# Kernel tuning notes

Measured on AMD Instinct MI355X. Metric: run time of the kernel, lower is better.

Reference implementation:

```python
import jax, jax.numpy as jnp
import numpy as np

N_HEAD = 16
D_HEAD = 64
D_MODEL = 1024
LN_EPS = 1e-5


def layer_norm(x, gamma, beta):
    mu = jnp.mean(x, axis=-1, keepdims=True)
    var = jnp.mean((x - mu) ** 2, axis=-1, keepdims=True)
    return (x - mu) * jax.lax.rsqrt(var + LN_EPS) * gamma + beta


def setup_inputs() -> dict:
    key = jax.random.key(0)
    ks = jax.random.split(key, 6)
    B, T = 2, 2048
    inp = jax.random.normal(ks[0], (B, T, D_MODEL), dtype=jnp.float32)
    # qkv_net: Linear(d_model, 3*n_head*d_head)
    W_qkv = jax.random.normal(ks[1], (3 * N_HEAD * D_HEAD, D_MODEL), dtype=jnp.float32) * (D_MODEL ** -0.5)
    b_qkv = jax.random.normal(ks[2], (3 * N_HEAD * D_HEAD,), dtype=jnp.float32) * 0.02
    # o_net: Linear(n_head*d_head, d_model, bias=False)
    W_o = jax.random.normal(ks[3], (D_MODEL, N_HEAD * D_HEAD), dtype=jnp.float32) * ((N_HEAD * D_HEAD) ** -0.5)
    gamma = jnp.ones((D_MODEL,), dtype=jnp.float32)
    beta = jnp.zeros((D_MODEL,), dtype=jnp.float32)
    return {"inp": inp, "W_qkv": W_qkv, "b_qkv": b_qkv, "W_o": W_o, "gamma": gamma, "beta": beta}


def reference(inp, W_qkv, b_qkv, W_o, gamma, beta):
    B, T, D = inp.shape
    H, dh = N_HEAD, D_HEAD
    scale = 1.0 / (dh ** 0.5)

    qkv = inp @ W_qkv.T + b_qkv                      # (B, T, 3*H*dh)
    head_q, head_k, head_v = jnp.split(qkv, 3, axis=2)
    # (B, T, H, dh) -> (B, H, T, dh)
    q = head_q.reshape(B, T, H, dh).transpose(0, 2, 1, 3)
    k = head_k.reshape(B, T, H, dh).transpose(0, 2, 1, 3)
    v = head_v.reshape(B, T, H, dh).transpose(0, 2, 1, 3)

    attn_score = jnp.einsum('bhqd,bhkd->bhqk', q, k) * scale  # (B, H, T, T)
    attn_prob = jax.nn.softmax(attn_score, axis=-1)           # dropatt is identity in eval
    attn_vec = jnp.einsum('bhqk,bhkd->bhqd', attn_prob, v)    # (B, H, T, dh)

    # Faithful to original: (B*H, T, dh) batch-major buffer is VIEWED as (H, B, T, dh)
    attn_vec = attn_vec.reshape(H, B, T, dh)
    attn_vec = attn_vec.transpose(1, 2, 0, 3).reshape(B, T, H * dh)

    attn_out = attn_vec @ W_o.T                                # dropout identity in eval
    return layer_norm(inp + attn_out, gamma, beta)
```

## Files before the change

### kernel.cpp

```cpp
#include <hip/hip_runtime.h>
#include <hip/hip_bf16.h>
#include <stdint.h>

typedef __bf16 bf16_t;
typedef __bf16 bf16x8 __attribute__((ext_vector_type(8)));
typedef __bf16 bf16x4 __attribute__((ext_vector_type(4)));
typedef float floatx4 __attribute__((ext_vector_type(4)));

#define QSCALE 0.180336879f

__device__ static inline void gll16(const void* g, void* l) {
    __builtin_amdgcn_global_load_lds((const __attribute__((address_space(1))) void*)g,
                                     (__attribute__((address_space(3))) void*)l, 16, 0, 0);
}

__global__ __launch_bounds__(256) void cvt_all(const float* __restrict__ inp,
                                               const float* __restrict__ wqkv,
                                               const float* __restrict__ wo,
                                               bf16_t* __restrict__ o_inp,
                                               bf16_t* __restrict__ o_wqkv,
                                               bf16_t* __restrict__ o_wo) {
    int blk = blockIdx.x;
    const float* src;
    bf16_t* dst;
    if (blk < 4096)      { src = inp;  dst = o_inp; }
    else if (blk < 7168) { src = wqkv; dst = o_wqkv; blk -= 4096; }
    else                 { src = wo;   dst = o_wo;   blk -= 7168; }
    int i = blk * 256 + threadIdx.x;
    float4 v = ((const float4*)src)[i];
    bf16x4 o;
    o[0] = (bf16_t)v.x; o[1] = (bf16_t)v.y; o[2] = (bf16_t)v.z; o[3] = (bf16_t)v.w;
    ((bf16x4*)dst)[i] = o;
}

__global__ __launch_bounds__(256, 3)
void gemm_qkv(const bf16_t* __restrict__ A, const bf16_t* __restrict__ Bw,
              const float* __restrict__ bias,
              bf16_t* __restrict__ qk, bf16_t* __restrict__ vT) {
    constexpr int K = 1024;
    __shared__ bf16_t lA[128 * 32];
    __shared__ bf16_t lB[128 * 32];
    const int tid  = threadIdx.x;
    const int lane = tid & 63, wave = tid >> 6;
    const int quad = lane >> 4, l16 = lane & 15;
    const int wy = wave >> 1, wx = wave & 1;
    const int bm = blockIdx.y * 128, bn = blockIdx.x * 128;

    const int c0 = tid, c1 = tid + 256;
    const bf16_t* Ap0 = A + (size_t)(bm + (c0 >> 2)) * K + (c0 & 3) * 8;
    const bf16_t* Ap1 = A + (size_t)(bm + (c1 >> 2)) * K + (c1 & 3) * 8;
    const bf16_t* Bp0 = Bw + (size_t)(bn + (c0 >> 2)) * K + (c0 & 3) * 8;
    const bf16_t* Bp1 = Bw + (size_t)(bn + (c1 >> 2)) * K + (c1 & 3) * 8;
    bf16_t* dA0 = &lA[(wave * 64) * 8];
    bf16_t* dA1 = &lA[(256 + wave * 64) * 8];
    bf16_t* dB0 = &lB[(wave * 64) * 8];
    bf16_t* dB1 = &lB[(256 + wave * 64) * 8];

    floatx4 acc[4][4] = {};

    for (int kt = 0; kt < K; kt += 32) {
        __syncthreads();
        gll16(Ap0 + kt, dA0);
        gll16(Ap1 + kt, dA1);
        gll16(Bp0 + kt, dB0);
        gll16(Bp1 + kt, dB1);
        __syncthreads();
        bf16x8 af[4], bfr[4];
#pragma unroll
        for (int i = 0; i < 4; i++) {
            af[i]  = *(const bf16x8*)(lA + (wy * 64 + i * 16 + l16) * 32 + quad * 8);
            bfr[i] = *(const bf16x8*)(lB + (wx * 64 + i * 16 + l16) * 32 + quad * 8);
        }
#pragma unroll
        for (int i = 0; i < 4; i++)
#pragma unroll
            for (int j = 0; j < 4; j++)
                acc[i][j] = __builtin_amdgcn_mfma_f32_16x16x32_bf16(af[i], bfr[j], acc[i][j], 0, 0, 0);
    }

    const bool is_v = (bn >= 2048);
#pragma unroll
    for (int j = 0; j < 4; j++) {
        const int n = bn + wx * 64 + j * 16 + l16;
        const float bv = bias[n];
        const bool isq = (n < 1024);
#pragma unroll
        for (int i = 0; i < 4; i++) {
            const int mbase = bm + wy * 64 + i * 16 + quad * 4;
            if (!is_v) {
#pragma unroll
                for (int r = 0; r < 4; r++) {
                    float c = acc[i][j][r] + bv;
                    if (isq) c *= QSCALE;
                    qk[(size_t)(mbase + r) * 2048 + n] = (bf16_t)c;
                }
            } else {
                const int nn = n - 2048;
                const int b  = mbase >> 11;
                const int t  = mbase & 2047;
                const int vrow = b * 1024 + nn;
                bf16x4 pack;
#pragma unroll
                for (int r = 0; r < 4; r++) pack[r] = (bf16_t)(acc[i][j][r] + bv);
                *(bf16x4*)(vT + (size_t)vrow * 2048 + t) = pack;
            }
        }
    }
}

__global__ __launch_bounds__(256, 3)
void attn_kernel(const bf16_t* __restrict__ qk, const bf16_t* __restrict__ vT,
                 bf16_t* __restrict__ av) {
    __shared__ bf16_t Kbuf[2][2][64 * 32];
    __shared__ bf16_t Vbuf[2][2][64 * 32];
    __shared__ bf16_t Pbuf[4][2][16 * 32];
    const int tid  = threadIdx.x;
    const int lane = tid & 63, wave = tid >> 6;
    const int quad = lane >> 4, l16 = lane & 15;
    const int bid = blockIdx.x;
    const int s  = bid & 31;
    const int hl = (s & 7) * 4 + (s >> 3);
    const int qt = bid >> 5;
    const int b = hl >> 4, h = hl & 15;

    const bf16_t* Qbase = qk + (size_t)(b * 2048 + qt * 128 + wave * 32) * 2048 + h * 64;
    const bf16_t* Kbase = qk + (size_t)(b * 2048) * 2048 + 1024 + h * 64;
    const bf16_t* Vbase = vT + (size_t)(hl * 64) * 2048;

    const int sr = tid >> 3;
    const int c8 = tid & 7;
    const int half = c8 >> 2, ce = (c8 & 3) * 8;
    const bf16_t* Kg = Kbase + (size_t)sr * 2048 + c8 * 8;
    const bf16_t* Vg = Vbase + (size_t)sr * 2048 + c8 * 8;

    bf16x8 qf[2][2];
#pragma unroll
    for (int rt = 0; rt < 2; rt++)
#pragma unroll
        for (int kc = 0; kc < 2; kc++)
            qf[rt][kc] = *(const bf16x8*)(Qbase + (size_t)(rt * 16 + l16) * 2048 + kc * 32 + quad * 8);

    floatx4 accO[2][4] = {};
    float lacc[2] = {0.f, 0.f};

    {
        bf16x8 k0 = *(const bf16x8*)(Kg);
        bf16x8 k1 = *(const bf16x8*)(Kg + (size_t)32 * 2048);
        bf16x8 v0 = *(const bf16x8*)(Vg);
        bf16x8 v1 = *(const bf16x8*)(Vg + (size_t)32 * 2048);
        *(bf16x8*)&Kbuf[0][half][sr * 32 + ce] = k0;
        *(bf16x8*)&Kbuf[0][half][(sr + 32) * 32 + ce] = k1;
        *(bf16x8*)&Vbuf[0][half][sr * 32 + ce] = v0;
        *(bf16x8*)&Vbuf[0][half][(sr + 32) * 32 + ce] = v1;
    }

    for (int it = 0; it < 32; ++it) {
        const int cur = it & 1;
        __syncthreads();
        bf16x8 gk0, gk1, gv0, gv1;
        if (it < 31) {
            const bf16_t* kg = Kg + (size_t)(it + 1) * 64 * 2048;
            const bf16_t* vg = Vg + (it + 1) * 64;
            gk0 = *(const bf16x8*)(kg);
            gk1 = *(const bf16x8*)(kg + (size_t)32 * 2048);
            gv0 = *(const bf16x8*)(vg);
            gv1 = *(const bf16x8*)(vg + (size_t)32 * 2048);
        }
        floatx4 st[2][4] = {};
#pragma unroll
        for (int nt = 0; nt < 4; nt++) {
            bf16x8 k0 = *(const bf16x8*)&Kbuf[cur][0][(nt * 16 + l16) * 32 + quad * 8];
            bf16x8 k1 = *(const bf16x8*)&Kbuf[cur][1][(nt * 16 + l16) * 32 + quad * 8];
            st[0][nt] = __builtin_amdgcn_mfma_f32_16x16x32_bf16(k0, qf[0][0], st[0][nt], 0, 0, 0);
            st[0][nt] = __builtin_amdgcn_mfma_f32_16x16x32_bf16(k1, qf[0][1], st[0][nt], 0, 0, 0);
            st[1][nt] = __builtin_amdgcn_mfma_f32_16x16x32_bf16(k0, qf[1][0], st[1][nt], 0, 0, 0);
            st[1][nt] = __builtin_amdgcn_mfma_f32_16x16x32_bf16(k1, qf[1][1], st[1][nt], 0, 0, 0);
        }
#pragma unroll
        for (int rt = 0; rt < 2; rt++) {
            float ls = 0.f;
#pragma unroll
            for (int nt = 0; nt < 4; nt++) {
                bf16x4 pk;
#pragma unroll
                for (int r = 0; r < 4; r++) {
                    float p = __builtin_amdgcn_exp2f(st[rt][nt][r]);
                    ls += p;
                    pk[r] = (bf16_t)p;
                }
                *(bf16x4*)&Pbuf[wave][nt >> 1][l16 * 32 + (nt & 1) * 16 + quad * 4] = pk;
            }
            lacc[rt] += ls;
        }
#pragma unroll
        for (int kc2 = 0; kc2 < 2; kc2++) {
            bf16x8 pf0 = *(const bf16x8*)&Pbuf[wave][kc2][l16 * 32 + quad * 8];
            pf0 = pf0;
            break;
        }
        {
#pragma unroll
            for (int rt = 0; rt < 2; rt++) {
#pragma unroll
                for (int nt = 0; nt < 4; nt++) {
                    bf16x4 pk;
#pragma unroll
                    for (int r = 0; r < 4; r++)
                        pk[r] = (bf16_t)__builtin_amdgcn_exp2f(st[rt][nt][r]);
                    *(bf16x4*)&Pbuf[wave][nt >> 1][l16 * 32 + (nt & 1) * 16 + quad * 4] = pk;
                }
#pragma unroll
                for (int kc2 = 0; kc2 < 2; kc2++) {
                    bf16x8 pf = *(const bf16x8*)&Pbuf[wave][kc2][l16 * 32 + quad * 8];
#pragma unroll
                    for (int ct = 0; ct < 4; ct++) {
                        bf16x8 vf = *(const bf16x8*)&Vbuf[cur][kc2][(ct * 16 + l16) * 32 + quad * 8];
                        accO[rt][ct] = __builtin_amdgcn_mfma_f32_16x16x32_bf16(pf, vf, accO[rt][ct], 0, 0, 0);
                    }
                }
            }
        }
        if (it < 31) {
            const int nxt = cur ^ 1;
            *(bf16x8*)&Kbuf[nxt][half][sr * 32 + ce] = gk0;
            *(bf16x8*)&Kbuf[nxt][half][(sr + 32) * 32 + ce] = gk1;
            *(bf16x8*)&Vbuf[nxt][half][sr * 32 + ce] = gv0;
            *(bf16x8*)&Vbuf[nxt][half][(sr + 32) * 32 + ce] = gv1;
        }
    }

    float linv[2];
#pragma unroll
    for (int rt = 0; rt < 2; rt++) {
        float l = lacc[rt];
        l += __shfl_xor(l, 16);
        l += __shfl_xor(l, 32);
        linv[rt] = 1.0f / l;
    }
    const int b2 = hl & 1;
    const int colb = (hl >> 1) * 64;
    bf16_t* outb = av + (size_t)(b2 * 2048 + qt * 128 + wave * 32) * 1024 + colb;
#pragma unroll
    for (int rt = 0; rt < 2; rt++) {
        float invq[4];
#pragma unroll
        for (int r = 0; r < 4; r++) invq[r] = __shfl(linv[rt], quad * 4 + r);
#pragma unroll
        for (int ct = 0; ct < 4; ct++)
#pragma unroll
            for (int r = 0; r < 4; r++)
                outb[(size_t)(rt * 16 + quad * 4 + r) * 1024 + ct * 16 + l16] =
                    (bf16_t)(accO[rt][ct][r] * invq[r]);
    }
}

__global__ __launch_bounds__(256, 4)
void gemm_o(const bf16_t* __restrict__ A, const bf16_t* __restrict__ Bw,
            float* __restrict__ out) {
    constexpr int K = 1024;
    __shared__ bf16_t lA[64 * 32];
    __shared__ bf16_t lB[128 * 32];
    const int tid  = threadIdx.x;
    const int lane = tid & 63, wave = tid >> 6;
    const int quad = lane >> 4, l16 = lane & 15;
    const int wy = wave >> 1, wx = wave & 1;
    const int bm = blockIdx.y * 64, bn = blockIdx.x * 128;

    const int ca = tid;
    const int cb0 = tid, cb1 = tid + 256;
    const bf16_t* Ap  = A + (size_t)(bm + (ca >> 2)) * K + (ca & 3) * 8;
    const bf16_t* Bp0 = Bw + (size_t)(bn + (cb0 >> 2)) * K + (cb0 & 3) * 8;
    const bf16_t* Bp1 = Bw + (size_t)(bn + (cb1 >> 2)) * K + (cb1 & 3) * 8;
    bf16_t* dA  = &lA[(wave * 64) * 8];
    bf16_t* dB0 = &lB[(wave * 64) * 8];
    bf16_t* dB1 = &lB[(256 + wave * 64) * 8];

    floatx4 acc[2][4] = {};
    for (int kt = 0; kt < K; kt += 32) {
        __syncthreads();
        gll16(Ap + kt, dA);
        gll16(Bp0 + kt, dB0);
        gll16(Bp1 + kt, dB1);
        __syncthreads();
        bf16x8 af[2], bfr[4];
#pragma unroll
        for (int i = 0; i < 2; i++)
            af[i] = *(const bf16x8*)(lA + (wy * 32 + i * 16 + l16) * 32 + quad * 8);
#pragma unroll
        for (int j = 0; j < 4; j++)
            bfr[j] = *(const bf16x8*)(lB + (wx * 64 + j * 16 + l16) * 32 + quad * 8);
#pragma unroll
        for (int i = 0; i < 2; i++)
#pragma unroll
            for (int j = 0; j < 4; j++)
                acc[i][j] = __builtin_amdgcn_mfma_f32_16x16x32_bf16(af[i], bfr[j], acc[i][j], 0, 0, 0);
    }
#pragma unroll
    for (int j = 0; j < 4; j++) {
        const int n = bn + wx * 64 + j * 16 + l16;
#pragma unroll
        for (int i = 0; i < 2; i++) {
            const int mbase = bm + wy * 32 + i * 16 + quad * 4;
#pragma unroll
            for (int r = 0; r < 4; r++)
                out[(size_t)(mbase + r) * 1024 + n] = acc[i][j][r];
        }
    }
}

__global__ __launch_bounds__(256)
void ln_kernel(const float* __restrict__ inp, const float* __restrict__ ao,
               const float* __restrict__ gamma, const float* __restrict__ beta,
               float* __restrict__ out) {
    const int row = blockIdx.x, tid = threadIdx.x;
    const int wave = tid >> 6, lane = tid & 63;
    float4 a = ((const float4*)(inp + (size_t)row * 1024))[tid];
    float4 c = ((const float4*)(ao + (size_t)row * 1024))[tid];
    float x0 = a.x + c.x, x1 = a.y + c.y, x2 = a.z + c.z, x3 = a.w + c.w;
    float s = x0 + x1 + x2 + x3;
    float sq = x0 * x0 + x1 * x1 + x2 * x2 + x3 * x3;
#pragma unroll
    for (int mm = 32; mm >= 1; mm >>= 1) {
        s += __shfl_xor(s, mm);
        sq += __shfl_xor(sq, mm);
    }
    __shared__ float rs[4], rq[4];
    if (lane == 0) { rs[wave] = s; rq[wave] = sq; }
    __syncthreads();
    s = rs[0] + rs[1] + rs[2] + rs[3];
    sq = rq[0] + rq[1] + rq[2] + rq[3];
    const float mu = s * (1.0f / 1024.0f);
    const float var = sq * (1.0f / 1024.0f) - mu * mu;
    const float rstd = rsqrtf(var + 1e-5f);
    float4 g = ((const float4*)gamma)[tid], bt = ((const float4*)beta)[tid];
    float4 o;
    o.x = (x0 - mu) * rstd * g.x + bt.x;
    o.y = (x1 - mu) * rstd * g.y + bt.y;
    o.z = (x2 - mu) * rstd * g.z + bt.z;
    o.w = (x3 - mu) * rstd * g.w + bt.w;
    ((float4*)(out + (size_t)row * 1024))[tid] = o;
}

extern "C" void kernel_launch(void* const* d_in, const int* in_sizes, int n_in,
                              void* d_out, int out_size, void* d_ws, size_t ws_size,
                              hipStream_t stream) {
    const float* inp   = (const float*)d_in[0];
    const float* Wqkv  = (const float*)d_in[1];
    const float* bqkv  = (const float*)d_in[2];
    const float* Wo    = (const float*)d_in[3];
    const float* gamma = (const float*)d_in[4];
    const float* beta  = (const float*)d_in[5];
    float* out = (float*)d_out;

    char* ws = (char*)d_ws;
    bf16_t* inp_bf  = (bf16_t*)(ws);
    bf16_t* wqkv_bf = (bf16_t*)(ws + (8u << 20));
    bf16_t* wo_bf   = (bf16_t*)(ws + (14u << 20));
    bf16_t* qk_buf  = (bf16_t*)(ws + (16u << 20));
    bf16_t* vT_buf  = (bf16_t*)(ws + (32u << 20));
    bf16_t* av_buf  = (bf16_t*)(ws + (40u << 20));
    float*  ao_buf  = (float*)(ws + (48u << 20));

    cvt_all<<<8192, 256, 0, stream>>>(inp, Wqkv, Wo, inp_bf, wqkv_bf, wo_bf);
    gemm_qkv<<<dim3(24, 32), 256, 0, stream>>>(inp_bf, wqkv_bf, bqkv, qk_buf, vT_buf);
    attn_kernel<<<512, 256, 0, stream>>>(qk_buf, vT_buf, av_buf);
    gemm_o<<<dim3(8, 64), 256, 0, stream>>>(av_buf, wo_bf, ao_buf);
    ln_kernel<<<4096, 256, 0, stream>>>(inp, ao_buf, gamma, beta, out);
}
```

Before: 210.4 us.

## Split attention over key halves with global_load_lds staging and combine kernel

The attention kernel now splits the key dimension into two halves, doubling the grid to 1024 blocks. Each block writes an unnormalized partial output and row sums, and a new combine kernel adds the halves and normalizes. K/V tiles are staged with direct global-to-LDS loads instead of register round-trips, the duplicated exp/P recomputation is removed, and the occupancy hint is raised to 4. The cost is an extra kernel launch plus partial-buffer traffic, and workspace regions are reused (lpart over inp_bf, opart over ao_buf).

```diff
diff --git a/kernel.cpp b/kernel.cpp
--- a/kernel.cpp
+++ b/kernel.cpp
@@ -108,30 +108,33 @@
     }
 }
 
-__global__ __launch_bounds__(256, 3)
+__global__ __launch_bounds__(256, 4)
 void attn_kernel(const bf16_t* __restrict__ qk, const bf16_t* __restrict__ vT,
-                 bf16_t* __restrict__ av) {
-    __shared__ bf16_t Kbuf[2][2][64 * 32];
-    __shared__ bf16_t Vbuf[2][2][64 * 32];
-    __shared__ bf16_t Pbuf[4][2][16 * 32];
+                 bf16_t* __restrict__ Opart, float* __restrict__ lpart) {
+    __shared__ bf16_t Kbuf[2][64 * 64];
+    __shared__ bf16_t Vbuf[2][64 * 64];
+    __shared__ bf16_t Pbuf[4][16 * 32];
     const int tid  = threadIdx.x;
     const int lane = tid & 63, wave = tid >> 6;
     const int quad = lane >> 4, l16 = lane & 15;
     const int bid = blockIdx.x;
-    const int s  = bid & 31;
-    const int hl = (s & 7) * 4 + (s >> 3);
-    const int qt = bid >> 5;
+    const int s    = bid & 63;
+    const int hl   = ((s & 7) << 2) | ((s >> 3) & 3);
+    const int half = (s >> 5) & 1;
+    const int qt   = bid >> 6;
     const int b = hl >> 4, h = hl & 15;
+    const int kt0 = half * 1024;
 
     const bf16_t* Qbase = qk + (size_t)(b * 2048 + qt * 128 + wave * 32) * 2048 + h * 64;
     const bf16_t* Kbase = qk + (size_t)(b * 2048) * 2048 + 1024 + h * 64;
     const bf16_t* Vbase = vT + (size_t)(hl * 64) * 2048;
 
-    const int sr = tid >> 3;
-    const int c8 = tid & 7;
-    const int half = c8 >> 2, ce = (c8 & 3) * 8;
-    const bf16_t* Kg = Kbase + (size_t)sr * 2048 + c8 * 8;
-    const bf16_t* Vg = Vbase + (size_t)sr * 2048 + c8 * 8;
+    const int srow = tid >> 2, sc8 = (tid & 3) * 8;
+    const bf16_t* KgA = Kbase + (size_t)(kt0 + srow) * 2048 + sc8;
+    const bf16_t* KgB = KgA + 32;
+    const bf16_t* VgA = Vbase + (size_t)srow * 2048 + kt0 + sc8;
+    const bf16_t* VgB = VgA + 32;
+    const int wbase = wave * 512;
 
     bf16x8 qf[2][2];
 #pragma unroll
@@ -143,115 +146,102 @@
     floatx4 accO[2][4] = {};
     float lacc[2] = {0.f, 0.f};
 
-    {
-        bf16x8 k0 = *(const bf16x8*)(Kg);
-        bf16x8 k1 = *(const bf16x8*)(Kg + (size_t)32 * 2048);
-        bf16x8 v0 = *(const bf16x8*)(Vg);
-        bf16x8 v1 = *(const bf16x8*)(Vg + (size_t)32 * 2048);
-        *(bf16x8*)&Kbuf[0][half][sr * 32 + ce] = k0;
-        *(bf16x8*)&Kbuf[0][half][(sr + 32) * 32 + ce] = k1;
-        *(bf16x8*)&Vbuf[0][half][sr * 32 + ce] = v0;
-        *(bf16x8*)&Vbuf[0][half][(sr + 32) * 32 + ce] = v1;
-    }
-
-    for (int it = 0; it < 32; ++it) {
-        const int cur = it & 1;
-        __syncthreads();
-        bf16x8 gk0, gk1, gv0, gv1;
-        if (it < 31) {
-            const bf16_t* kg = Kg + (size_t)(it + 1) * 64 * 2048;
-            const bf16_t* vg = Vg + (it + 1) * 64;
-            gk0 = *(const bf16x8*)(kg);
-            gk1 = *(const bf16x8*)(kg + (size_t)32 * 2048);
-            gv0 = *(const bf16x8*)(vg);
-            gv1 = *(const bf16x8*)(vg + (size_t)32 * 2048);
+    gll16(KgA, &Kbuf[0][wbase]);
+    gll16(KgB, &Kbuf[0][2048 + wbase]);
+    gll16(VgA, &Vbuf[0][wbase]);
+    gll16(VgB, &Vbuf[0][2048 + wbase]);
+
+    for (int it = 0; it < 16; ++it) {
+        const int cur = it & 1, nxt = cur ^ 1;
+        __syncthreads();
+        if (it < 15) {
+            const size_t ko = (size_t)(it + 1) * 64 * 2048;
+            const int    vo = (it + 1) * 64;
+            gll16(KgA + ko, &Kbuf[nxt][wbase]);
+            gll16(KgB + ko, &Kbuf[nxt][2048 + wbase]);
+            gll16(VgA + vo, &Vbuf[nxt][wbase]);
+            gll16(VgB + vo, &Vbuf[nxt][2048 + wbase]);
         }
         floatx4 st[2][4] = {};
 #pragma unroll
         for (int nt = 0; nt < 4; nt++) {
-            bf16x8 k0 = *(const bf16x8*)&Kbuf[cur][0][(nt * 16 + l16) * 32 + quad * 8];
-            bf16x8 k1 = *(const bf16x8*)&Kbuf[cur][1][(nt * 16 + l16) * 32 + quad * 8];
+            bf16x8 k0 = *(const bf16x8*)&Kbuf[cur][(nt * 16 + l16) * 32 + quad * 8];
+            bf16x8 k1 = *(const bf16x8*)&Kbuf[cur][2048 + (nt * 16 + l16) * 32 + quad * 8];
             st[0][nt] = __builtin_amdgcn_mfma_f32_16x16x32_bf16(k0, qf[0][0], st[0][nt], 0, 0, 0);
             st[0][nt] = __builtin_amdgcn_mfma_f32_16x16x32_bf16(k1, qf[0][1], st[0][nt], 0, 0, 0);
             st[1][nt] = __builtin_amdgcn_mfma_f32_16x16x32_bf16(k0, qf[1][0], st[1][nt], 0, 0, 0);
             st[1][nt] = __builtin_amdgcn_mfma_f32_16x16x32_bf16(k1, qf[1][1], st[1][nt], 0, 0, 0);
         }
 #pragma unroll
-        for (int rt = 0; rt < 2; rt++) {
-            float ls = 0.f;
-#pragma unroll
-            for (int nt = 0; nt < 4; nt++) {
-                bf16x4 pk;
-#pragma unroll
-                for (int r = 0; r < 4; r++) {
-                    float p = __builtin_amdgcn_exp2f(st[rt][nt][r]);
-                    ls += p;
-                    pk[r] = (bf16_t)p;
+        for (int kc2 = 0; kc2 < 2; kc2++) {
+            bf16x8 vf[4];
+#pragma unroll
+            for (int ct = 0; ct < 4; ct++)
+                vf[ct] = *(const bf16x8*)&Vbuf[cur][kc2 * 2048 + (ct * 16 + l16) * 32 + quad * 8];
+#pragma unroll
+            for (int rt = 0; rt < 2; rt++) {
+                float ls = 0.f;
+#pragma unroll
+                for (int ntl = 0; ntl < 2; ntl++) {
+                    const floatx4 sv = st[rt][kc2 * 2 + ntl];
+                    bf16x4 pk;
+#pragma unroll
+                    for (int r = 0; r < 4; r++) {
+                        float p = __builtin_amdgcn_exp2f(sv[r]);
+                        ls += p;
+                        pk[r] = (bf16_t)p;
+                    }
+                    *(bf16x4*)&Pbuf[wave][l16 * 32 + ntl * 16 + quad * 4] = pk;
                 }
-                *(bf16x4*)&Pbuf[wave][nt >> 1][l16 * 32 + (nt & 1) * 16 + quad * 4] = pk;
+                lacc[rt] += ls;
+                bf16x8 pf = *(const bf16x8*)&Pbuf[wave][l16 * 32 + quad * 8];
+#pragma unroll
+                for (int ct = 0; ct < 4; ct++)
+                    accO[rt][ct] = __builtin_amdgcn_mfma_f32_16x16x32_bf16(pf, vf[ct], accO[rt][ct], 0, 0, 0);
             }
-            lacc[rt] += ls;
-        }
-#pragma unroll
-        for (int kc2 = 0; kc2 < 2; kc2++) {
-            bf16x8 pf0 = *(const bf16x8*)&Pbuf[wave][kc2][l16 * 32 + quad * 8];
-            pf0 = pf0;
-            break;
-        }
-        {
-#pragma unroll
-            for (int rt = 0; rt < 2; rt++) {
-#pragma unroll
-                for (int nt = 0; nt < 4; nt++) {
-                    bf16x4 pk;
-#pragma unroll
-                    for (int r = 0; r < 4; r++)
-                        pk[r] = (bf16_t)__builtin_amdgcn_exp2f(st[rt][nt][r]);
-                    *(bf16x4*)&Pbuf[wave][nt >> 1][l16 * 32 + (nt & 1) * 16 + quad * 4] = pk;
-                }
-#pragma unroll
-                for (int kc2 = 0; kc2 < 2; kc2++) {
-                    bf16x8 pf = *(const bf16x8*)&Pbuf[wave][kc2][l16 * 32 + quad * 8];
-#pragma unroll
-                    for (int ct = 0; ct < 4; ct++) {
-                        bf16x8 vf = *(const bf16x8*)&Vbuf[cur][kc2][(ct * 16 + l16) * 32 + quad * 8];
-                        accO[rt][ct] = __builtin_amdgcn_mfma_f32_16x16x32_bf16(pf, vf, accO[rt][ct], 0, 0, 0);
-                    }
-                }
-            }
-        }
-        if (it < 31) {
-            const int nxt = cur ^ 1;
-            *(bf16x8*)&Kbuf[nxt][half][sr * 32 + ce] = gk0;
-            *(bf16x8*)&Kbuf[nxt][half][(sr + 32) * 32 + ce] = gk1;
-            *(bf16x8*)&Vbuf[nxt][half][sr * 32 + ce] = gv0;
-            *(bf16x8*)&Vbuf[nxt][half][(sr + 32) * 32 + ce] = gv1;
-        }
-    }
-
-    float linv[2];
+        }
+    }
+
+    float lsum[2];
 #pragma unroll
     for (int rt = 0; rt < 2; rt++) {
         float l = lacc[rt];
         l += __shfl_xor(l, 16);
         l += __shfl_xor(l, 32);
-        linv[rt] = 1.0f / l;
+        lsum[rt] = l;
     }
     const int b2 = hl & 1;
-    const int colb = (hl >> 1) * 64;
-    bf16_t* outb = av + (size_t)(b2 * 2048 + qt * 128 + wave * 32) * 1024 + colb;
-#pragma unroll
-    for (int rt = 0; rt < 2; rt++) {
-        float invq[4];
-#pragma unroll
-        for (int r = 0; r < 4; r++) invq[r] = __shfl(linv[rt], quad * 4 + r);
+    const int colb = hl >> 1;
+    const int rowb = b2 * 2048 + qt * 128 + wave * 32;
+    bf16_t* outb = Opart + (size_t)half * (4096 * 1024) + (size_t)rowb * 1024 + colb * 64;
+#pragma unroll
+    for (int rt = 0; rt < 2; rt++)
 #pragma unroll
         for (int ct = 0; ct < 4; ct++)
 #pragma unroll
             for (int r = 0; r < 4; r++)
-                outb[(size_t)(rt * 16 + quad * 4 + r) * 1024 + ct * 16 + l16] =
-                    (bf16_t)(accO[rt][ct][r] * invq[r]);
-    }
+                outb[(size_t)(rt * 16 + quad * 4 + r) * 1024 + ct * 16 + l16] = (bf16_t)(accO[rt][ct][r]);
+    if (quad == 0) {
+#pragma unroll
+        for (int rt = 0; rt < 2; rt++)
+            lpart[half * 65536 + (rowb + rt * 16 + l16) * 16 + colb] = lsum[rt];
+    }
+}
+
+__global__ __launch_bounds__(256)
+void attn_combine(const bf16_t* __restrict__ Op, const float* __restrict__ lp,
+                  bf16_t* __restrict__ av) {
+    const int row = blockIdx.x, tid = threadIdx.x;
+    const int col = tid * 4, cb = col >> 6;
+    const float l = lp[row * 16 + cb] + lp[65536 + row * 16 + cb];
+    const float inv = 1.0f / l;
+    bf16x4 o0 = *(const bf16x4*)(Op + (size_t)row * 1024 + col);
+    bf16x4 o1 = *(const bf16x4*)(Op + (size_t)(4096 + row) * 1024 + col);
+    bf16x4 o;
+#pragma unroll
+    for (int i = 0; i < 4; i++)
+        o[i] = (bf16_t)(((float)o0[i] + (float)o1[i]) * inv);
+    *(bf16x4*)(av + (size_t)row * 1024 + col) = o;
 }
 
 __global__ __launch_bounds__(256, 4)
@@ -360,10 +350,13 @@
     bf16_t* vT_buf  = (bf16_t*)(ws + (32u << 20));
     bf16_t* av_buf  = (bf16_t*)(ws + (40u << 20));
     float*  ao_buf  = (float*)(ws + (48u << 20));
+    bf16_t* opart   = (bf16_t*)(ws + (48u << 20));
+    float*  lpart   = (float*)(ws);
 
     cvt_all<<<8192, 256, 0, stream>>>(inp, Wqkv, Wo, inp_bf, wqkv_bf, wo_bf);
     gemm_qkv<<<dim3(24, 32), 256, 0, stream>>>(inp_bf, wqkv_bf, bqkv, qk_buf, vT_buf);
-    attn_kernel<<<512, 256, 0, stream>>>(qk_buf, vT_buf, av_buf);
+    attn_kernel<<<1024, 256, 0, stream>>>(qk_buf, vT_buf, opart, lpart);
+    attn_combine<<<4096, 256, 0, stream>>>(opart, lpart, av_buf);
     gemm_o<<<dim3(8, 64), 256, 0, stream>>>(av_buf, wo_bf, ao_buf);
     ln_kernel<<<4096, 256, 0, stream>>>(inp, ao_buf, gamma, beta, out);
 }
```

After: 216.0 us. +2.7%, slower.
